# Performance work log

Measured on AMD Instinct MI355X. Metric: run time of the kernel, lower is better.

Reference implementation:

```python
import jax, jax.numpy as jnp
import numpy as np

D_MODEL = 768
D_STATE = 16
EXPAND = 2
D_INNER = D_MODEL * EXPAND
K_CONV = 4
RMS_EPS = 1.1920928955078125e-07  # torch.finfo(float32).eps (nn.RMSNorm default eps=None)


def setup_inputs() -> dict:
    key = jax.random.key(0)
    ks = jax.random.split(key, 8)
    x = jax.random.normal(ks[0], (2, 2048, D_MODEL), dtype=jnp.float32)
    # parameters (torch Linear stores [out, in]; we keep that layout and use x @ W.T)
    in_proj_w = jax.random.normal(ks[1], (2 * D_INNER, D_MODEL), jnp.float32) * (1.0 / np.sqrt(D_MODEL))
    conv_w = jax.random.normal(ks[2], (D_INNER, 1, K_CONV), jnp.float32) * (1.0 / np.sqrt(K_CONV))
    conv_b = jax.random.normal(ks[3], (D_INNER,), jnp.float32) * 0.1
    x_proj_w = jax.random.normal(ks[4], (2 * D_STATE, D_INNER), jnp.float32) * (1.0 / np.sqrt(D_INNER))
    dt_proj_w = jax.random.normal(ks[5], (D_INNER, D_INNER), jnp.float32) * (1.0 / np.sqrt(D_INNER))
    dt_proj_b = jax.random.normal(ks[6], (D_INNER,), jnp.float32) * 0.1
    A_log = jnp.log(jnp.broadcast_to(jnp.arange(1, D_STATE + 1, dtype=jnp.float32)[None, :], (D_INNER, D_STATE)))
    D_skip = jnp.ones((D_INNER,), jnp.float32)
    out_proj_w = jax.random.normal(ks[7], (D_MODEL, D_INNER), jnp.float32) * (1.0 / np.sqrt(D_INNER))
    norm_w = jnp.ones((D_MODEL,), jnp.float32)
    return {"x": x, "norm_w": norm_w, "in_proj_w": in_proj_w, "conv_w": conv_w,
            "conv_b": conv_b, "x_proj_w": x_proj_w, "dt_proj_w": dt_proj_w,
            "dt_proj_b": dt_proj_b, "A_log": A_log, "D_skip": D_skip,
            "out_proj_w": out_proj_w}


def reference(x, norm_w, in_proj_w, conv_w, conv_b, x_proj_w, dt_proj_w,
              dt_proj_b, A_log, D_skip, out_proj_w):
    # x: [B, L, d_model]
    residual = x
    xn = x * jax.lax.rsqrt(jnp.mean(x * x, axis=-1, keepdims=True) + RMS_EPS) * norm_w
    xz = xn @ in_proj_w.T                       # [B, L, 2*d_inner]
    d_inner = in_proj_w.shape[0] // 2
    xb, z = xz[..., :d_inner], xz[..., d_inner:]
    # causal depthwise conv: torch pads 3 both sides then truncates to L == left-pad 3
    xc = jax.lax.conv_general_dilated(
        xb.transpose(0, 2, 1), conv_w, window_strides=(1,), padding=[(K_CONV - 1, 0)],
        feature_group_count=d_inner, dimension_numbers=("NCH", "OIH", "NCH"))
    xc = xc + conv_b[None, :, None]
    u = jax.nn.silu(xc.transpose(0, 2, 1))      # [B, L, d_inner]
    bc = u @ x_proj_w.T                          # [B, L, 2*d_state]
    N = A_log.shape[1]
    Bp, Cp = bc[..., :N], bc[..., N:]
    delta = jax.nn.softplus(u @ dt_proj_w.T + dt_proj_b)  # [B, L, d_inner]
    A = -jnp.exp(A_log)                          # [d_inner, N]

    def step(h, ins):
        dl, ut, Bt, Ct = ins                     # [B,D], [B,D], [B,N], [B,N]
        dA = jnp.exp(dl[:, :, None] * A)         # [B, D, N]
        h = dA * h + dl[:, :, None] * Bt[:, None, :] * ut[:, :, None]
        y = jnp.einsum("bdn,bn->bd", h, Ct)
        return h, y

    B_, L, _ = u.shape
    h0 = jnp.zeros((B_, d_inner, N), x.dtype)
    xs = (delta.transpose(1, 0, 2), u.transpose(1, 0, 2),
          Bp.transpose(1, 0, 2), Cp.transpose(1, 0, 2))
    _, ys = jax.lax.scan(step, h0, xs)           # ys: [L, B, d_inner]
    y = ys.transpose(1, 0, 2) + u * D_skip
    out = (y * jax.nn.silu(z)) @ out_proj_w.T
    return out + residual
```

## Files before the change

### kernel.cpp

```cpp
#include <hip/hip_runtime.h>
#include <math.h>

#define DM 768
#define DI 1536
#define NS 16
#define LL 2048
#define MROWS 4096
#define CH 32
#define NC 64

using bf16x8 = __attribute__((ext_vector_type(8))) short;
using f32x4 = __attribute__((ext_vector_type(4))) float;

__device__ __forceinline__ float4 ld4(const float* p) { return *(const float4*)p; }

__device__ __forceinline__ unsigned short f2bf(float f) {
  unsigned int u = __float_as_uint(f);
  u += 0x7fff + ((u >> 16) & 1);
  return (unsigned short)(u >> 16);
}
__device__ __forceinline__ float b2f(unsigned short s) {
  return __uint_as_float(((unsigned int)s) << 16);
}

__device__ __forceinline__ void gload16(const void* g, void* l) {
  __builtin_amdgcn_global_load_lds((const __attribute__((address_space(1))) void*)g,
                                   (__attribute__((address_space(3))) void*)l, 16, 0, 0);
}

#define N4_IN 589824
#define N4_CAT 638976
#define N4_OUT 294912
__global__ __launch_bounds__(256) void cvt_all(const float* __restrict__ ipw,
                                               const float* __restrict__ dtw,
                                               const float* __restrict__ xpw,
                                               const float* __restrict__ opw,
                                               unsigned short* __restrict__ d_in4,
                                               unsigned short* __restrict__ d_cat,
                                               unsigned short* __restrict__ d_out4) {
  int i = blockIdx.x * 256 + threadIdx.x;
  if (i < N4_IN) {
    float4 v = ld4(ipw + (size_t)i * 4);
    ushort4 o = {f2bf(v.x), f2bf(v.y), f2bf(v.z), f2bf(v.w)};
    *(ushort4*)(d_in4 + (size_t)i * 4) = o;
  } else if (i < N4_IN + N4_CAT) {
    int j = i - N4_IN;
    int row = j / 384;
    int col = (j % 384) * 4;
    ushort4 o = {0, 0, 0, 0};
    if (row < 1536) {
      float4 v = ld4(dtw + (size_t)row * DI + col);
      o = {f2bf(v.x), f2bf(v.y), f2bf(v.z), f2bf(v.w)};
    } else if (row < 1568) {
      float4 v = ld4(xpw + (size_t)(row - 1536) * DI + col);
      o = {f2bf(v.x), f2bf(v.y), f2bf(v.z), f2bf(v.w)};
    }
    *(ushort4*)(d_cat + (size_t)j * 4) = o;
  } else if (i < N4_IN + N4_CAT + N4_OUT) {
    int j = i - N4_IN - N4_CAT;
    float4 v = ld4(opw + (size_t)j * 4);
    ushort4 o = {f2bf(v.x), f2bf(v.y), f2bf(v.z), f2bf(v.w)};
    *(ushort4*)(d_out4 + (size_t)j * 4) = o;
  }
}

__global__ __launch_bounds__(256) void rmsnorm_kernel(const float* __restrict__ x,
                                                      const float* __restrict__ w,
                                                      unsigned short* __restrict__ xn) {
  int row = blockIdx.x;
  const float* xr = x + (size_t)row * DM;
  unsigned short* xo = xn + (size_t)row * DM;
  int tid = threadIdx.x;
  float v0 = xr[tid], v1 = xr[tid + 256], v2 = xr[tid + 512];
  float ss = v0 * v0 + v1 * v1 + v2 * v2;
#pragma unroll
  for (int o = 32; o > 0; o >>= 1) ss += __shfl_xor(ss, o, 64);
  __shared__ float red[4];
  if ((tid & 63) == 0) red[tid >> 6] = ss;
  __syncthreads();
  float tot = red[0] + red[1] + red[2] + red[3];
  float sc = rsqrtf(tot * (1.0f / 768.0f) + 1.1920928955078125e-07f);
  xo[tid] = f2bf(v0 * sc * w[tid]);
  xo[tid + 256] = f2bf(v1 * sc * w[tid + 256]);
  xo[tid + 512] = f2bf(v2 * sc * w[tid + 512]);
}

template <int EPI, int BM, int BN>
__global__ __launch_bounds__(256) void mfma_gemm(const unsigned short* __restrict__ A,
                                                 const unsigned short* __restrict__ Bw,
                                                 const float* __restrict__ bias,
                                                 const float* __restrict__ resid,
                                                 void* __restrict__ o0v,
                                                 void* __restrict__ o1v, int K, int gx) {
  constexpr int NFI = BM / 32;
  constexpr int NFJ = BN / 32;
  constexpr int NCH = (BM + BN) / 8;
  __shared__ unsigned short As[BM * 64];
  __shared__ unsigned short Bs[BN * 64];
  int tid = threadIdx.x;
  int lane = tid & 63, w = tid >> 6;
  int wr = w >> 1, wc = w & 1;

  int nwg = gx * gridDim.y;
  int orig = blockIdx.y * gx + blockIdx.x;
  int q = nwg >> 3;
  int swz = (orig & 7) * q + (orig >> 3);
  int bm = (swz / gx) * BM, bn = (swz % gx) * BN;

  f32x4 acc[NFI][NFJ];
#pragma unroll
  for (int i = 0; i < NFI; i++)
#pragma unroll
    for (int j = 0; j < NFJ; j++) acc[i][j] = (f32x4){0.f, 0.f, 0.f, 0.f};

  const unsigned short* Ab = A + (size_t)bm * K;
  const unsigned short* Bb = Bw + (size_t)bn * K;
  int lrow = lane >> 3;
  int kof = ((lane & 7) ^ lrow) * 8;

  auto stage = [&](int k0) {
#pragma unroll
    for (int ch = w; ch < NCH; ch += 4) {
      if (ch < BM / 8) {
        int row = ch * 8 + lrow;
        gload16(Ab + (size_t)row * K + k0 + kof, &As[ch * 512]);
      } else {
        int row = (ch - BM / 8) * 8 + lrow;
        gload16(Bb + (size_t)row * K + k0 + kof, &Bs[(ch - BM / 8) * 512]);
      }
    }
  };
  auto compute = [&]() {
#pragma unroll
    for (int kk = 0; kk < 2; kk++) {
      int sa = (((kk * 4) + (lane >> 4)) ^ (lane & 7)) * 8;
      bf16x8 af[NFI], bfr[NFJ];
#pragma unroll
      for (int i = 0; i < NFI; i++) {
        int arow = wr * (BM / 2) + i * 16 + (lane & 15);
        af[i] = *(const bf16x8*)&As[arow * 64 + sa];
      }
#pragma unroll
      for (int j = 0; j < NFJ; j++) {
        int brow = wc * (BN / 2) + j * 16 + (lane & 15);
        bfr[j] = *(const bf16x8*)&Bs[brow * 64 + sa];
      }
#pragma unroll
      for (int i = 0; i < NFI; i++)
#pragma unroll
        for (int j = 0; j < NFJ; j++)
          acc[i][j] = __builtin_amdgcn_mfma_f32_16x16x32_bf16(af[i], bfr[j], acc[i][j], 0, 0, 0);
    }
  };

  int nk = K >> 6;
  for (int t = 0; t < nk; t++) {
    __syncthreads();
    stage(t << 6);
    __syncthreads();
    compute();
  }

#pragma unroll
  for (int i = 0; i < NFI; i++) {
#pragma unroll
    for (int j = 0; j < NFJ; j++) {
      int row0 = bm + wr * (BM / 2) + i * 16 + (lane >> 4) * 4;
      int col = bn + wc * (BN / 2) + j * 16 + (lane & 15);
#pragma unroll
      for (int r = 0; r < 4; r++) {
        float v = acc[i][j][r];
        int row = row0 + r;
        if (EPI == 0) {
          unsigned short* xb = (unsigned short*)o0v;
          unsigned short* z = (unsigned short*)o1v;
          if (col < DI) xb[(size_t)row * DI + col] = f2bf(v);
          else z[(size_t)row * DI + col - DI] = f2bf(v);
        } else if (EPI == 1) {
          float* delta = (float*)o0v;
          float* bc = (float*)o1v;
          if (col < DI) {
            v += bias[col];
            v = (v > 20.0f) ? v : log1pf(expf(v));
            delta[(size_t)row * DI + col] = v;
          } else if (col < DI + 2 * NS) {
            bc[(size_t)row * 32 + col - DI] = v;
          }
        } else {
          float* out = (float*)o0v;
          out[(size_t)row * DM + col] = v + resid[(size_t)row * DM + col];
        }
      }
    }
  }
}

__global__ __launch_bounds__(192) void conv_silu_kernel(const unsigned short* __restrict__ xb,
                                                        const float* __restrict__ cw,
                                                        const float* __restrict__ cb,
                                                        unsigned short* __restrict__ u) {
  int d = (blockIdx.x * 192 + threadIdx.x) << 2;
  int m = blockIdx.y;
  int t = m & (LL - 1);
  float4 w0 = ld4(cw + d * 4);
  float4 w1 = ld4(cw + d * 4 + 4);
  float4 w2 = ld4(cw + d * 4 + 8);
  float4 w3 = ld4(cw + d * 4 + 12);
  float4 acc = {cb[d], cb[d + 1], cb[d + 2], cb[d + 3]};
#pragma unroll
  for (int tap = 0; tap < 4; tap++) {
    int dt_ = 3 - tap;
    if (t >= dt_) {
      ushort4 xv = *(const ushort4*)(xb + (size_t)(m - dt_) * DI + d);
      float wx = (tap == 0) ? w0.x : (tap == 1) ? w0.y : (tap == 2) ? w0.z : w0.w;
      float wy = (tap == 0) ? w1.x : (tap == 1) ? w1.y : (tap == 2) ? w1.z : w1.w;
      float wz = (tap == 0) ? w2.x : (tap == 1) ? w2.y : (tap == 2) ? w2.z : w2.w;
      float ww = (tap == 0) ? w3.x : (tap == 1) ? w3.y : (tap == 2) ? w3.z : w3.w;
      acc.x += b2f(xv.x) * wx;
      acc.y += b2f(xv.y) * wy;
      acc.z += b2f(xv.z) * wz;
      acc.w += b2f(xv.w) * ww;
    }
  }
  ushort4 o = {f2bf(acc.x / (1.0f + __expf(-acc.x))), f2bf(acc.y / (1.0f + __expf(-acc.y))),
               f2bf(acc.z / (1.0f + __expf(-acc.z))), f2bf(acc.w / (1.0f + __expf(-acc.w)))};
  *(ushort4*)(u + (size_t)m * DI + d) = o;
}

__global__ __launch_bounds__(256) void scan_pass1(const float* __restrict__ delta,
                                                  const unsigned short* __restrict__ u,
                                                  const float* __restrict__ bc,
                                                  const float* __restrict__ A_log,
                                                  float* __restrict__ chunkP,
                                                  float* __restrict__ chunkS) {
  int d = blockIdx.x * 256 + threadIdx.x;
  int c = blockIdx.y;
  int b = blockIdx.z;
  float Acoef[NS];
#pragma unroll
  for (int n = 0; n < NS; n++) Acoef[n] = -__expf(A_log[d * NS + n]);
  __shared__ float sB[CH][NS];
  const float* bcb = bc + (size_t)(b * LL + c * CH) * 32;
  for (int i = threadIdx.x; i < CH * NS; i += 256) sB[i >> 4][i & 15] = bcb[(i >> 4) * 32 + (i & 15)];
  __syncthreads();
  float P[NS], S[NS];
#pragma unroll
  for (int n = 0; n < NS; n++) { P[n] = 1.f; S[n] = 0.f; }
  int m0 = b * LL + c * CH;
  for (int tt = 0; tt < CH; tt++) {
    size_t off = (size_t)(m0 + tt) * DI + d;
    float dl = delta[off];
    float ut = b2f(u[off]);
    float dlu = dl * ut;
#pragma unroll
    for (int n = 0; n < NS; n++) {
      float dA = __expf(dl * Acoef[n]);
      S[n] = dA * S[n] + dlu * sB[tt][n];
      P[n] *= dA;
    }
  }
  size_t base = ((size_t)(b * NC + c) * NS) * DI + d;
#pragma unroll
  for (int n = 0; n < NS; n++) {
    chunkP[base + (size_t)n * DI] = P[n];
    chunkS[base + (size_t)n * DI] = S[n];
  }
}

__global__ __launch_bounds__(256) void scan_pass2(const float* __restrict__ chunkP,
                                                  float* __restrict__ chunkS) {
  int id = blockIdx.x * 256 + threadIdx.x;
  int d = id % DI;
  int n = (id / DI) % NS;
  int b = id / (DI * NS);
  float h = 0.f;
  for (int c = 0; c < NC; c++) {
    size_t idx = ((size_t)(b * NC + c) * NS + n) * DI + d;
    float p = chunkP[idx];
    float s = chunkS[idx];
    chunkS[idx] = h;
    h = p * h + s;
  }
}

__global__ __launch_bounds__(256) void scan_pass3(const float* __restrict__ delta,
                                                  const unsigned short* __restrict__ u,
                                                  const float* __restrict__ bc,
                                                  const float* __restrict__ hIn,
                                                  const float* __restrict__ A_log,
                                                  const float* __restrict__ D_skip,
                                                  const unsigned short* __restrict__ z,
                                                  unsigned short* __restrict__ yg) {
  int d = blockIdx.x * 256 + threadIdx.x;
  int c = blockIdx.y;
  int b = blockIdx.z;
  float Acoef[NS];
#pragma unroll
  for (int n = 0; n < NS; n++) Acoef[n] = -__expf(A_log[d * NS + n]);
  float Dsk = D_skip[d];
  __shared__ float sBC[CH][32];
  const float* bcb = bc + (size_t)(b * LL + c * CH) * 32;
  for (int i = threadIdx.x; i < CH * 32; i += 256) sBC[i >> 5][i & 31] = bcb[i];
  __syncthreads();
  float h[NS];
  size_t base = ((size_t)(b * NC + c) * NS) * DI + d;
#pragma unroll
  for (int n = 0; n < NS; n++) h[n] = hIn[base + (size_t)n * DI];
  int m0 = b * LL + c * CH;
  for (int tt = 0; tt < CH; tt++) {
    size_t m = (size_t)(m0 + tt);
    size_t off = m * DI + d;
    float dl = delta[off];
    float ut = b2f(u[off]);
    float dlu = dl * ut;
    float yt = 0.f;
#pragma unroll
    for (int n = 0; n < NS; n++) {
      float dA = __expf(dl * Acoef[n]);
      h[n] = dA * h[n] + dlu * sBC[tt][n];
      yt += h[n] * sBC[tt][16 + n];
    }
    float zv = b2f(z[m * DI + d]);
    float sz = zv / (1.0f + __expf(-zv));
    yg[m * DI + d] = f2bf((yt + ut * Dsk) * sz);
  }
}

extern "C" void kernel_launch(void* const* d_in, const int* in_sizes, int n_in,
                              void* d_out, int out_size, void* d_ws, size_t ws_size,
                              hipStream_t stream) {
  const float* x = (const float*)d_in[0];
  const float* norm_w = (const float*)d_in[1];
  const float* in_proj_w = (const float*)d_in[2];
  const float* conv_w = (const float*)d_in[3];
  const float* conv_b = (const float*)d_in[4];
  const float* x_proj_w = (const float*)d_in[5];
  const float* dt_proj_w = (const float*)d_in[6];
  const float* dt_proj_b = (const float*)d_in[7];
  const float* A_log = (const float*)d_in[8];
  const float* D_skip = (const float*)d_in[9];
  const float* out_proj_w = (const float*)d_in[10];
  float* out = (float*)d_out;

  float* ws = (float*)d_ws;
  unsigned short* xb_bf = (unsigned short*)ws;
  unsigned short* z_bf = (unsigned short*)(ws + 3145728);
  unsigned short* u_bf = (unsigned short*)(ws + 6291456);
  float* delta = ws + 9437184;
  unsigned short* ygbf = (unsigned short*)(ws + 15728640);
  unsigned short* wbf_in = (unsigned short*)(ws + 18874368);
  unsigned short* wbf_cat = (unsigned short*)(ws + 20054016);
  unsigned short* wbf_out = (unsigned short*)(ws + 21331968);
  float* chunkP = ws + 21921792;
  float* chunkS = ws + 25067520;
  unsigned short* xn_bf = (unsigned short*)d_out;
  float* bcb = (float*)d_out + 1572864;

  cvt_all<<<5953, 256, 0, stream>>>(in_proj_w, dt_proj_w, x_proj_w, out_proj_w,
                                    wbf_in, wbf_cat, wbf_out);

  rmsnorm_kernel<<<4096, 256, 0, stream>>>(x, norm_w, xn_bf);

  mfma_gemm<0, 64, 128><<<dim3(24, 64), 256, 0, stream>>>(xn_bf, wbf_in, nullptr, nullptr,
                                                          xb_bf, z_bf, DM, 24);

  conv_silu_kernel<<<dim3(2, 4096), 192, 0, stream>>>(xb_bf, conv_w, conv_b, u_bf);

  mfma_gemm<1, 64, 64><<<dim3(26, 64), 256, 0, stream>>>(u_bf, wbf_cat, dt_proj_b, nullptr,
                                                         delta, bcb, DI, 26);

  scan_pass1<<<dim3(6, NC, 2), 256, 0, stream>>>(delta, u_bf, bcb, A_log, chunkP, chunkS);
  scan_pass2<<<192, 256, 0, stream>>>(chunkP, chunkS);
  scan_pass3<<<dim3(6, NC, 2), 256, 0, stream>>>(delta, u_bf, bcb, chunkS, A_log, D_skip,
                                                 z_bf, ygbf);

  mfma_gemm<2, 64, 64><<<dim3(12, 64), 256, 0, stream>>>(ygbf, wbf_out, nullptr, x, out,
                                                         nullptr, DI, 12);
}
```

Before: 219.9 us.

## Double-buffer LDS tiles in MFMA GEMM and shrink in_proj tile to 64x64

The bf16 MFMA GEMM now keeps two LDS buffers for A and B. It prefetches the next K-tile with async global-to-LDS loads while computing on the current one, using s_waitcnt vmcnt and raw barriers instead of two __syncthreads per iteration. The in_proj GEMM moves from a 64x128 to a 64x64 tile with twice as many blocks, so every instance issues four loads per wave, which is what the hardcoded vmcnt(4) assumes. This doubles LDS use per block and ties correctness to that fixed per-wave load count.

Measured after the change: 223.6 us. Within noise of the previous version (+1.7%).

```diff
diff --git a/kernel.cpp b/kernel.cpp
--- a/kernel.cpp
+++ b/kernel.cpp
@@ -95,8 +95,8 @@
   constexpr int NFI = BM / 32;
   constexpr int NFJ = BN / 32;
   constexpr int NCH = (BM + BN) / 8;
-  __shared__ unsigned short As[BM * 64];
-  __shared__ unsigned short Bs[BN * 64];
+  __shared__ unsigned short As[2][BM * 64];
+  __shared__ unsigned short Bs[2][BN * 64];
   int tid = threadIdx.x;
   int lane = tid & 63, w = tid >> 6;
   int wr = w >> 1, wc = w & 1;
@@ -118,19 +118,19 @@
   int lrow = lane >> 3;
   int kof = ((lane & 7) ^ lrow) * 8;
 
-  auto stage = [&](int k0) {
+  auto stage = [&](int buf, int k0) {
 #pragma unroll
     for (int ch = w; ch < NCH; ch += 4) {
       if (ch < BM / 8) {
         int row = ch * 8 + lrow;
-        gload16(Ab + (size_t)row * K + k0 + kof, &As[ch * 512]);
+        gload16(Ab + (size_t)row * K + k0 + kof, &As[buf][ch * 512]);
       } else {
         int row = (ch - BM / 8) * 8 + lrow;
-        gload16(Bb + (size_t)row * K + k0 + kof, &Bs[(ch - BM / 8) * 512]);
+        gload16(Bb + (size_t)row * K + k0 + kof, &Bs[buf][(ch - BM / 8) * 512]);
       }
     }
   };
-  auto compute = [&]() {
+  auto compute = [&](int buf) {
 #pragma unroll
     for (int kk = 0; kk < 2; kk++) {
       int sa = (((kk * 4) + (lane >> 4)) ^ (lane & 7)) * 8;
@@ -138,12 +138,12 @@
 #pragma unroll
       for (int i = 0; i < NFI; i++) {
         int arow = wr * (BM / 2) + i * 16 + (lane & 15);
-        af[i] = *(const bf16x8*)&As[arow * 64 + sa];
+        af[i] = *(const bf16x8*)&As[buf][arow * 64 + sa];
       }
 #pragma unroll
       for (int j = 0; j < NFJ; j++) {
         int brow = wc * (BN / 2) + j * 16 + (lane & 15);
-        bfr[j] = *(const bf16x8*)&Bs[brow * 64 + sa];
+        bfr[j] = *(const bf16x8*)&Bs[buf][brow * 64 + sa];
       }
 #pragma unroll
       for (int i = 0; i < NFI; i++)
@@ -154,11 +154,17 @@
   };
 
   int nk = K >> 6;
+  stage(0, 0);
   for (int t = 0; t < nk; t++) {
-    __syncthreads();
-    stage(t << 6);
-    __syncthreads();
-    compute();
+    if (t + 1 < nk) {
+      stage((t + 1) & 1, (t + 1) << 6);
+      asm volatile("s_waitcnt vmcnt(4)" ::: "memory");
+    } else {
+      asm volatile("s_waitcnt vmcnt(0)" ::: "memory");
+    }
+    __builtin_amdgcn_s_barrier();
+    compute(t & 1);
+    __builtin_amdgcn_s_barrier();
   }
 
 #pragma unroll
@@ -361,8 +367,8 @@
 
   rmsnorm_kernel<<<4096, 256, 0, stream>>>(x, norm_w, xn_bf);
 
-  mfma_gemm<0, 64, 128><<<dim3(24, 64), 256, 0, stream>>>(xn_bf, wbf_in, nullptr, nullptr,
-                                                          xb_bf, z_bf, DM, 24);
+  mfma_gemm<0, 64, 64><<<dim3(48, 64), 256, 0, stream>>>(xn_bf, wbf_in, nullptr, nullptr,
+                                                         xb_bf, z_bf, DM, 48);
 
   conv_silu_kernel<<<dim3(2, 4096), 192, 0, stream>>>(xb_bf, conv_w, conv_b, u_bf);
 
```
